# Performance work log

Hardware: AMD Instinct MI355X
Metric: run time of the kernel (lower is better)

Reference implementation:

```python
import jax, jax.numpy as jnp
import numpy as np

LMAX = 3
L2 = (LMAX + 1) ** 2
EPS = 1e-5
N_NODES = 2048
C_IN = 384
C_HID = 256


def _gaunt_tensor(lmax):
    # Real Gaunt coefficients G[i,j,k] = integral Y_i Y_j Y_k dOmega over S^2,
    # computed exactly with Gauss-Legendre (theta) x uniform (phi) quadrature.
    nt = 4 * lmax + 4
    nph = 8 * lmax + 8
    xg, wg = np.polynomial.legendre.leggauss(nt)
    ct, st = xg, np.sqrt(1.0 - xg ** 2)
    phi = 2.0 * np.pi * np.arange(nph) / nph
    # fully-normalized associated Legendre Pbar[l,m] on theta nodes
    P = np.zeros((lmax + 1, lmax + 1, nt))
    P[0, 0] = np.sqrt(1.0 / (4.0 * np.pi))
    for m in range(1, lmax + 1):
        P[m, m] = np.sqrt((2.0 * m + 1.0) / (2.0 * m)) * st * P[m - 1, m - 1]
    for m in range(lmax + 1):
        if m + 1 <= lmax:
            P[m + 1, m] = np.sqrt(2.0 * m + 3.0) * ct * P[m, m]
        for l in range(m + 2, lmax + 1):
            a = np.sqrt((4.0 * l * l - 1.0) / (l * l - m * m))
            b = np.sqrt(((l - 1.0) ** 2 - m * m) / (4.0 * (l - 1.0) ** 2 - 1.0))
            P[l, m] = a * (ct * P[l - 1, m] - b * P[l - 2, m])
    Y = np.zeros(((lmax + 1) ** 2, nt, nph))
    for l in range(lmax + 1):
        for m in range(-l, l + 1):
            idx = l * l + l + m
            if m == 0:
                Y[idx] = P[l, 0][:, None] * np.ones((1, nph))
            elif m > 0:
                Y[idx] = np.sqrt(2.0) * P[l, m][:, None] * np.cos(m * phi)[None, :]
            else:
                Y[idx] = np.sqrt(2.0) * P[l, -m][:, None] * np.sin(-m * phi)[None, :]
    W = wg[:, None] * (2.0 * np.pi / nph)  # [nt, nph]
    G = np.einsum('iap,jap,kap->ijk', Y, Y, Y * W[None])
    G[np.abs(G) < 1e-10] = 0.0
    return G


G_NP = _gaunt_tensor(LMAX)
SL = [slice(l * l, (l + 1) * (l + 1)) for l in range(LMAX + 1)]
_raw = []
for _l1 in range(LMAX + 1):
    for _l2 in range(LMAX + 1):
        for _l3 in range(LMAX + 1):
            _blk = G_NP[SL[_l1], SL[_l2], SL[_l3]]
            if np.abs(_blk).max() > 1e-8:
                _raw.append((_l1, _l2, _l3, _blk))
_fanin = {}
for _l1, _l2, _l3, _b in _raw:
    _fanin[_l3] = _fanin.get(_l3, 0) + 1
# component irrep normalization (sqrt(2l3+1)) and path normalization (1/sqrt(fan-in))
PATHS = [(l1, l2, l3, jnp.asarray((blk * np.sqrt(2.0 * l3 + 1.0) / np.sqrt(_fanin[l3])).astype(np.float32)))
         for (l1, l2, l3, blk) in _raw]
L_OF = jnp.asarray(np.repeat(np.arange(LMAX + 1), 2 * np.arange(LMAX + 1) + 1))  # [L2]


def setup_inputs() -> dict:
    key = jax.random.key(0)
    ks = jax.random.split(key, 9)
    inputs = jax.random.normal(ks[0], (N_NODES, L2, C_IN), jnp.float32)
    batch = jnp.sort(jax.random.randint(ks[1], (N_NODES,), 0, 64))
    norm_w = 1.0 + 0.1 * jax.random.normal(ks[2], (LMAX + 1, C_IN), jnp.float32)
    norm_b = 0.02 * jax.random.normal(ks[3], (C_IN,), jnp.float32)
    w1 = jax.random.normal(ks[4], (LMAX + 1, C_IN, C_HID), jnp.float32) / np.sqrt(C_IN)
    b1 = 0.02 * jax.random.normal(ks[5], (C_HID,), jnp.float32)
    w_gaunt = jax.random.normal(ks[6], (LMAX + 1, LMAX + 1, LMAX + 1, C_HID), jnp.float32)
    w2 = jax.random.normal(ks[7], (LMAX + 1, C_HID, C_IN), jnp.float32) / np.sqrt(C_HID)
    b2 = 0.02 * jax.random.normal(ks[8], (C_IN,), jnp.float32)
    return {"inputs": inputs, "batch": batch, "norm_w": norm_w, "norm_b": norm_b,
            "w1": w1, "b1": b1, "w_gaunt": w_gaunt, "w2": w2, "b2": b2}


def _forward(inputs, norm_w, norm_b, w1, b1, w_gaunt, w2, b2):
    # equivariant merge layer norm: center l=0 over channels, RMS over all (lm, C),
    # per-degree affine weight, bias on the l=0 (invariant) component only
    x = inputs
    x = x.at[:, 0, :].add(-jnp.mean(x[:, 0, :], axis=-1, keepdims=True))
    x = x * jax.lax.rsqrt(jnp.mean(x * x, axis=(1, 2), keepdims=True) + EPS)
    x = x * norm_w[L_OF][None]          # [N, L2, C]
    x = x.at[:, 0, :].add(norm_b)
    # SO3Linear 1: per-degree channel mixing, bias on l=0
    h = jnp.einsum('nic,ich->nih', x, w1[L_OF])
    h = h.at[:, 0, :].add(b1)
    # Gaunt depthwise self tensor product: per-channel CG-structured contraction
    t = jnp.zeros((inputs.shape[0], L2, w1.shape[-1]), dtype=h.dtype)
    for (l1, l2, l3, blk) in PATHS:
        hw = h[:, SL[l2], :] * w_gaunt[l1, l2, l3][None, None, :]     # [N, 2l2+1, H]
        tmp = jnp.einsum('ijk,nih->njkh', blk, h[:, SL[l1], :])       # small block contraction
        t = t.at[:, SL[l3], :].add(jnp.einsum('njkh,njh->nkh', tmp, hw))
    # SO3Linear 2
    out = jnp.einsum('nih,iho->nio', t, w2[L_OF])
    out = out.at[:, 0, :].add(b2)
    return out + inputs  # ffn_shortcut is Identity (num_in == num_out)


def reference(inputs, batch, norm_w, norm_b, w1, b1, w_gaunt, w2, b2):
    # drop_path / proj_drop are disabled (rates = 0); `batch` only feeds GraphDropPath
    return _forward(inputs, norm_w, norm_b, w1, b1, w_gaunt, w2, b2)
```

## Files before the change

kernel.cpp:

```cpp
#include <hip/hip_runtime.h>
#include <stdint.h>
#include <math.h>
#include <array>
#include <utility>

#ifndef M_PI
#define M_PI 3.14159265358979323846
#endif

#define NNODES 2048
#define L2DIM  16
#define CIN    384
#define CHID   256

typedef __attribute__((ext_vector_type(8))) short short8;
typedef __attribute__((ext_vector_type(4))) float f32x4;
typedef unsigned short u16;
typedef unsigned int   u32;

#define LOF(i) ((i) < 1 ? 0 : ((i) < 4 ? 1 : ((i) < 9 ? 2 : 3)))

static __device__ __forceinline__ u16 f2bf(float f) {
  u32 u = __builtin_bit_cast(u32, f);
  u = u + 0x7FFFu + ((u >> 16) & 1u);
  return (u16)(u >> 16);
}
static __device__ __forceinline__ float bf2f(u16 b) {
  u32 u = ((u32)b) << 16;
  return __builtin_bit_cast(float, u);
}

constexpr double CPI = 3.14159265358979323846;

constexpr double csqrt(double x) {
  if (x <= 0.0) return 0.0;
  double y = x > 1.0 ? x : 1.0;
  for (int i = 0; i < 48; ++i) y = 0.5 * (y + x / y);
  return y;
}
constexpr double ccos(double x) {
  double r = x;
  while (r > CPI)  r -= 2.0 * CPI;
  while (r < -CPI) r += 2.0 * CPI;
  double r2 = r * r, term = 1.0, sum = 1.0;
  for (int i = 1; i <= 26; ++i) { term *= -r2 / ((2.0 * i - 1.0) * (2.0 * i)); sum += term; }
  return sum;
}
constexpr int iabs_c(int x) { return x < 0 ? -x : x; }

struct GLQ { double x[16]; double w[16]; };
constexpr GLQ build_gl() {
  GLQ g{};
  const int n = 16;
  for (int i = 0; i < n; ++i) {
    double x = ccos(CPI * (i + 0.75) / (n + 0.5));
    double p1 = 0.0, dp = 1.0;
    for (int it = 0; it < 40; ++it) {
      double p0 = 1.0; p1 = x;
      for (int k = 2; k <= n; ++k) { double p2 = ((2.0*k-1.0)*x*p1 - (k-1.0)*p0)/k; p0 = p1; p1 = p2; }
      dp = n * (x*p1 - p0) / (x*x - 1.0);
      x -= p1 / dp;
    }
    { double p0 = 1.0; p1 = x;
      for (int k = 2; k <= n; ++k) { double p2 = ((2.0*k-1.0)*x*p1 - (k-1.0)*p0)/k; p0 = p1; p1 = p2; }
      dp = n * (x*p1 - p0) / (x*x - 1.0); }
    g.x[i] = x;
    g.w[i] = 2.0 / ((1.0 - x*x) * dp * dp);
  }
  return g;
}
constexpr GLQ QG = build_gl();

struct PTab { double v[4][4][16]; };
constexpr PTab build_pbar() {
  PTab T{};
  for (int t = 0; t < 16; ++t) {
    double ct = QG.x[t];
    double st = csqrt(1.0 - ct * ct);
    double P[4][4] = {};
    P[0][0] = csqrt(1.0 / (4.0 * CPI));
    for (int m = 1; m <= 3; ++m)
      P[m][m] = csqrt((2.0*m + 1.0) / (2.0*m)) * st * P[m-1][m-1];
    for (int m = 0; m <= 3; ++m) {
      if (m + 1 <= 3) P[m+1][m] = csqrt(2.0*m + 3.0) * ct * P[m][m];
      for (int l = m + 2; l <= 3; ++l) {
        double aa = csqrt((4.0*(double)l*l - 1.0) / ((double)l*l - (double)m*m));
        double bb = csqrt(((double)(l-1)*(l-1) - (double)m*m) / (4.0*(double)(l-1)*(l-1) - 1.0));
        P[l][m] = aa * (ct * P[l-1][m] - bb * P[l-2][m]);
      }
    }
    for (int l = 0; l < 4; ++l)
      for (int m = 0; m <= l; ++m) T.v[l][m][t] = P[l][m];
  }
  return T;
}
constexpr PTab PT = build_pbar();

constexpr double phi_int(int m1, int m2, int m3) {
  const double SQ2 = 1.41421356237309504880;
  int neg = (m1 < 0) + (m2 < 0) + (m3 < 0);
  if (neg & 1) return 0.0;
  int a = iabs_c(m1), b = iabs_c(m2), c = iabs_c(m3);
  int nz = (a > 0) + (b > 0) + (c > 0);
  if (nz == 0) return 2.0 * CPI;
  if (nz == 1) return 0.0;
  if (nz == 2) {
    int p = 0, q = 0;
    if (a == 0) { p = b; q = c; } else if (b == 0) { p = a; q = c; } else { p = a; q = b; }
    return (p == q) ? 2.0 * CPI : 0.0;
  }
  if (neg == 0) {
    double v = 0.0;
    if (iabs_c(a - b) == c && a != b) v += 1.0;
    if (a + b == c) v += 1.0;
    return SQ2 * CPI * v;
  }
  int p = 0, q = 0, r = 0;
  if (m1 > 0)      { p = a; q = b; r = c; }
  else if (m2 > 0) { p = b; q = a; r = c; }
  else             { p = c; q = a; r = b; }
  double v = 0.0;
  if (q != r && p == iabs_c(q - r)) v += 1.0;
  if (p == q + r) v -= 1.0;
  return SQ2 * CPI * v;
}

constexpr bool path_ok(int l1, int l2, int l3) {
  int lo = l1 > l2 ? l1 - l2 : l2 - l1;
  return l3 >= lo && l3 <= l1 + l2 && (((l1 + l2 + l3) & 1) == 0);
}
constexpr bool term_ok(int m1, int m2, int m3) {
  int aa = iabs_c(m1), bb = iabs_c(m2), cc = iabs_c(m3);
  int neg = (m1 < 0) + (m2 < 0) + (m3 < 0);
  if (neg & 1) return false;
  return (aa + bb == cc) || (bb + cc == aa) || (cc + aa == bb);
}
constexpr int count_paths() {
  int n = 0;
  for (int l1 = 0; l1 < 4; ++l1) for (int l2 = 0; l2 < 4; ++l2) for (int l3 = 0; l3 < 4; ++l3)
    if (path_ok(l1, l2, l3)) ++n;
  return n;
}
constexpr int NPATHS = count_paths();
constexpr int NTMAX  = 512;

constexpr double term_g(int l1, int m1, int l2, int m2, int l3, int m3) {
  double ph = phi_int(m1, m2, m3);
  if (ph == 0.0) return 0.0;
  int a = iabs_c(m1), b = iabs_c(m2), c = iabs_c(m3);
  double s = 0.0;
  for (int t = 0; t < 16; ++t)
    s += QG.w[t] * PT.v[l1][a][t] * PT.v[l2][b][t] * PT.v[l3][c][t];
  double g = ph * s;
  double fan = (l3 == 0) ? 4.0 : (l3 == 1 ? 6.0 : (l3 == 2 ? 7.0 : 6.0));
  return g * csqrt((2.0 * (double)l3 + 1.0) / fan);
}

struct TermG { float g; unsigned char i, j, k, p; };
struct PathT { unsigned char l1, l2, l3; };
struct TGAll { TermG t[NTMAX]; int n; };
constexpr TGAll build_all() {
  TGAll r{};
  r.n = 0;
  int p = 0;
  for (int l1 = 0; l1 < 4; ++l1) for (int l2 = 0; l2 < 4; ++l2) for (int l3 = 0; l3 < 4; ++l3) {
    if (!path_ok(l1, l2, l3)) continue;
    for (int m1 = -l1; m1 <= l1; ++m1) for (int m2 = -l2; m2 <= l2; ++m2) for (int m3 = -l3; m3 <= l3; ++m3) {
      if (!term_ok(m1, m2, m3)) continue;
      double g = term_g(l1, m1, l2, m2, l3, m3);
      if (g > 1e-10 || g < -1e-10) {
        r.t[r.n].g = (float)g;
        r.t[r.n].i = (unsigned char)(l1 * l1 + l1 + m1);
        r.t[r.n].j = (unsigned char)(l2 * l2 + l2 + m2);
        r.t[r.n].k = (unsigned char)(l3 * l3 + l3 + m3);
        r.t[r.n].p = (unsigned char)p;
        ++r.n;
      }
    }
    ++p;
  }
  return r;
}
constexpr TGAll TGA = build_all();
constexpr int NNZ = TGA.n;

constexpr std::array<PathT, NPATHS> build_paths() {
  std::array<PathT, NPATHS> a{};
  int n = 0;
  for (int l1 = 0; l1 < 4; ++l1) for (int l2 = 0; l2 < 4; ++l2) for (int l3 = 0; l3 < 4; ++l3)
    if (path_ok(l1, l2, l3)) a[n++] = PathT{(unsigned char)l1, (unsigned char)l2, (unsigned char)l3};
  return a;
}
constexpr auto PATHS_ARR = build_paths();

template <size_t... Is>
__device__ __forceinline__ void gaunt_terms(std::index_sequence<Is...>,
    float* __restrict__ t, const float* __restrict__ h,
    const float* __restrict__ wgv) {
  ((t[TGA.t[Is].k] = fmaf(TGA.t[Is].g * wgv[TGA.t[Is].p],
                          h[TGA.t[Is].i] * h[TGA.t[Is].j],
                          t[TGA.t[Is].k])), ...);
}
template <size_t... Ps>
__device__ __forceinline__ void load_wgv(std::index_sequence<Ps...>,
    float* __restrict__ wgv, const float* __restrict__ wg, int c) {
  ((wgv[Ps] = wg[(size_t)(((int)PATHS_ARR[Ps].l1 * 4 + (int)PATHS_ARR[Ps].l2) * 4
                          + (int)PATHS_ARR[Ps].l3) * CHID + c]), ...);
}

__global__ __launch_bounds__(256) void prep_kernel(
    const float* __restrict__ x, const float* __restrict__ nw,
    const float* __restrict__ nb, u16* __restrict__ xnb,
    const float* __restrict__ w1, const float* __restrict__ w2,
    u16* __restrict__ w1t, u16* __restrict__ w2t) {
  int bid = blockIdx.x, tid = threadIdx.x;
  if (bid >= NNODES) {
    __shared__ float tile[32][33];
    int b2 = bid - NNODES;
    int z = b2 / 144, rem = b2 % 144;
    int by = rem / 12, bx = rem % 12;
    int R = z < 4 ? 384 : 256, C = z < 4 ? 256 : 384;
    int r0 = by * 32, c0 = bx * 32;
    if (r0 >= R || c0 >= C) return;
    const float* s = (z < 4 ? w1 : w2) + (size_t)(z & 3) * R * C;
    u16* d = (z < 4 ? w1t : w2t) + (size_t)(z & 3) * R * C;
    int tx = tid & 31, ty = tid >> 5;
    for (int rr = ty; rr < 32; rr += 8)
      tile[rr][tx] = s[(size_t)(r0 + rr) * C + (c0 + tx)];
    __syncthreads();
    for (int cc = ty; cc < 32; cc += 8)
      d[(size_t)(c0 + cc) * R + (r0 + tx)] = f2bf(tile[tx][cc]);
    return;
  }
  int n = bid;
  const float* xr = x + (size_t)n * (L2DIM * CIN);
  __shared__ float2 red[4];
  float4 v[6];
  float ssq = 0.f, m0p = 0.f;
#pragma unroll
  for (int q = 0; q < 6; ++q) {
    v[q] = reinterpret_cast<const float4*>(xr)[tid * 6 + q];
    ssq += v[q].x*v[q].x + v[q].y*v[q].y + v[q].z*v[q].z + v[q].w*v[q].w;
  }
  if (tid < 16) {
#pragma unroll
    for (int q = 0; q < 6; ++q) m0p += v[q].x + v[q].y + v[q].z + v[q].w;
  }
  float a = m0p, b = ssq;
#pragma unroll
  for (int off = 32; off > 0; off >>= 1) { a += __shfl_down(a, off, 64); b += __shfl_down(b, off, 64); }
  int lane = tid & 63, wid = tid >> 6;
  if (lane == 0) red[wid] = make_float2(a, b);
  __syncthreads();
  float sum0 = red[0].x + red[1].x + red[2].x + red[3].x;
  float ssqt = red[0].y + red[1].y + red[2].y + red[3].y;
  float mean0 = sum0 * (1.0f / CIN);
  float ss = ssqt - (float)CIN * mean0 * mean0;
  float rstd = rsqrtf(ss * (1.0f / (L2DIM * CIN)) + 1e-5f);

  int lm = tid >> 4;
  int l = LOF(lm);
  bool row0 = (lm == 0);
  int cbase = (tid & 15) * 24;
  u16* orow = xnb + (size_t)n * (L2DIM * CIN) + (size_t)tid * 24;
#pragma unroll
  for (int q = 0; q < 6; ++q) {
    int c = cbase + q * 4;
    float4 w4 = *reinterpret_cast<const float4*>(&nw[l * CIN + c]);
    float4 b4 = row0 ? *reinterpret_cast<const float4*>(&nb[c]) : make_float4(0,0,0,0);
    float sub = row0 ? mean0 : 0.f;
    float o0 = (v[q].x - sub) * rstd * w4.x + b4.x;
    float o1 = (v[q].y - sub) * rstd * w4.y + b4.y;
    float o2 = (v[q].z - sub) * rstd * w4.z + b4.z;
    float o3 = (v[q].w - sub) * rstd * w4.w + b4.w;
    ushort4 pk;
    pk.x = f2bf(o0); pk.y = f2bf(o1); pk.z = f2bf(o2); pk.w = f2bf(o3);
    *reinterpret_cast<ushort4*>(&orow[q * 4]) = pk;
  }
}

template <int KD, int ND, int BN, bool SECOND>
__global__ __launch_bounds__(512) void so3_gemm_kernel(
    const u16* __restrict__ A, const u16* __restrict__ BT,
    const float* __restrict__ bias, const float* __restrict__ resid,
    u16* __restrict__ outb, float* __restrict__ outf) {
  constexpr int NFRAG = BN / 64;
  constexpr int WN_T = BN / 4;
  constexpr int KT = KD / 64;
  static_assert((BN % 64) == 0 && NFRAG * 16 == WN_T, "");
  int l = blockIdx.z;
  int twol1 = 2 * l + 1;
  int mtiles = (NNODES * twol1) >> 6;
  if ((int)blockIdx.x >= mtiles) return;
  int col0 = blockIdx.y * BN;
  int tid = threadIdx.x, lane = tid & 63, wid = tid >> 6;
  int wm = wid >> 2, wn = wid & 3;

  __shared__ u16 Asm[2][64 * 64];
  __shared__ u16 Bsm[2][BN * 64];

  int ar = tid >> 3;
  const u16* asrc;
  {
    int Rg = blockIdx.x * 64 + ar;
    int node = Rg / twol1;
    int lm = l * l + (Rg - node * twol1);
    asrc = A + (size_t)(node * L2DIM + lm) * KD + ((tid & 7) ^ (ar & 7)) * 8;
  }
  const u16* bsrc[BN / 64];
#pragma unroll
  for (int i = 0; i < BN / 64; ++i) {
    int r = i * 64 + (tid >> 3);
    bsrc[i] = BT + (size_t)(l * ND + col0 + r) * KD + ((tid & 7) ^ (r & 7)) * 8;
  }

  auto stage = [&](int buf, int kt) {
    __builtin_amdgcn_global_load_lds(
        (const __attribute__((address_space(1))) void*)(asrc + kt * 64),
        (__attribute__((address_space(3))) void*)(&Asm[buf][wid * 512]),
        16, 0, 0);
#pragma unroll
    for (int i = 0; i < BN / 64; ++i)
      __builtin_amdgcn_global_load_lds(
          (const __attribute__((address_space(1))) void*)(bsrc[i] + kt * 64),
          (__attribute__((address_space(3))) void*)(&Bsm[buf][i * 4096 + wid * 512]),
          16, 0, 0);
  };

  f32x4 acc[2][NFRAG];
#pragma unroll
  for (int i = 0; i < 2; ++i)
#pragma unroll
    for (int j = 0; j < NFRAG; ++j) acc[i][j] = (f32x4){0.f, 0.f, 0.f, 0.f};

  stage(0, 0);
  __syncthreads();
#pragma unroll
  for (int kt = 0; kt < KT; ++kt) {
    int cur = kt & 1;
    if (kt + 1 < KT) stage(cur ^ 1, kt + 1);
#pragma unroll
    for (int ks = 0; ks < 2; ++ks) {
      short8 af[2], bfv[NFRAG];
#pragma unroll
      for (int mf = 0; mf < 2; ++mf) {
        int row = wm * 32 + mf * 16 + (lane & 15);
        int slot = (ks * 4 + (lane >> 4)) ^ (row & 7);
        af[mf] = *reinterpret_cast<const short8*>(&Asm[cur][row * 64 + slot * 8]);
      }
#pragma unroll
      for (int nf = 0; nf < NFRAG; ++nf) {
        int brow = wn * WN_T + nf * 16 + (lane & 15);
        int slot = (ks * 4 + (lane >> 4)) ^ (brow & 7);
        bfv[nf] = *reinterpret_cast<const short8*>(&Bsm[cur][brow * 64 + slot * 8]);
      }
#pragma unroll
      for (int mf = 0; mf < 2; ++mf)
#pragma unroll
        for (int nf = 0; nf < NFRAG; ++nf)
          acc[mf][nf] = __builtin_amdgcn_mfma_f32_16x16x32_bf16(af[mf], bfv[nf], acc[mf][nf], 0, 0, 0);
    }
    __syncthreads();
  }

#pragma unroll
  for (int mf = 0; mf < 2; ++mf) {
#pragma unroll
    for (int jj = 0; jj < 4; ++jj) {
      int Rg = blockIdx.x * 64 + wm * 32 + mf * 16 + (lane >> 4) * 4 + jj;
      int node = Rg / twol1;
      int lm = l * l + (Rg - node * twol1);
      size_t rowoff = (size_t)(node * L2DIM + lm);
#pragma unroll
      for (int nf = 0; nf < NFRAG; ++nf) {
        int colg = col0 + wn * WN_T + nf * 16 + (lane & 15);
        float vv = acc[mf][nf][jj];
        if (l == 0) vv += bias[colg];
        if (!SECOND) {
          outb[rowoff * ND + colg] = f2bf(vv);
        } else {
          outf[rowoff * ND + colg] = vv + resid[rowoff * ND + colg];
        }
      }
    }
  }
}

__global__ __launch_bounds__(256, 2) void gaunt_kernel(
    const u16* __restrict__ hb, const float* __restrict__ wg,
    u16* __restrict__ tb) {
  int n = blockIdx.x, c = threadIdx.x;
  const u16* hr = hb + (size_t)n * (L2DIM * CHID) + c;
  float h[16];
#pragma unroll
  for (int i = 0; i < 16; ++i) h[i] = bf2f(hr[i * CHID]);

  float wgv[NPATHS];
  load_wgv(std::make_index_sequence<NPATHS>{}, wgv, wg, c);

  float t[16];
#pragma unroll
  for (int k = 0; k < 16; ++k) t[k] = 0.f;

  gaunt_terms(std::make_index_sequence<NNZ>{}, t, h, wgv);

  u16* tr = tb + (size_t)n * (L2DIM * CHID) + c;
#pragma unroll
  for (int k = 0; k < 16; ++k) tr[k * CHID] = f2bf(t[k]);
}

extern "C" void kernel_launch(void* const* d_in, const int* in_sizes, int n_in,
                              void* d_out, int out_size, void* d_ws, size_t ws_size,
                              hipStream_t stream) {
  const float* inputs = (const float*)d_in[0];
  const float* norm_w = (const float*)d_in[2];
  const float* norm_b = (const float*)d_in[3];
  const float* w1     = (const float*)d_in[4];
  const float* b1     = (const float*)d_in[5];
  const float* wga    = (const float*)d_in[6];
  const float* w2     = (const float*)d_in[7];
  const float* b2     = (const float*)d_in[8];
  float* out = (float*)d_out;

  uint8_t* ws = (uint8_t*)d_ws;
  u16*   w1t = (u16*)(ws + 16384);
  u16*   w2t = (u16*)(ws + 802816);
  u16*   xnb = (u16*)(ws + 1589248);
  u16*   tb  = xnb;
  u16*   hb  = (u16*)(ws + 26755072);

  prep_kernel<<<NNODES + 1152, 256, 0, stream>>>(
      inputs, norm_w, norm_b, xnb, w1, w2, w1t, w2t);
  so3_gemm_kernel<CIN, CHID, 256, false><<<dim3(224, 1, 4), 512, 0, stream>>>(
      xnb, w1t, b1, nullptr, hb, nullptr);
  gaunt_kernel<<<NNODES, 256, 0, stream>>>(hb, wga, tb);
  so3_gemm_kernel<CHID, CIN, 192, true><<<dim3(224, 2, 4), 512, 0, stream>>>(
      tb, w2t, b2, inputs, nullptr, out);
}
```

Baseline: 86.82 us.

## Stage GEMM epilogue through LDS for vectorized stores; widen gaunt to two channels

The GEMM epilogue now writes accumulators into an LDS tile that reuses the staging buffers, then each thread writes contiguous row segments with 16-byte vector stores, adding the bias and residual as float4 values. The old epilogue issued scattered 2- or 4-byte stores. Separately, the gaunt kernel now processes two channels per thread with 32-bit loads and stores and float2 weight loads, which halves the grid. This cuts the number of memory transactions at the cost of one extra barrier, more LDS in the epilogue, and higher register pressure in the gaunt kernel (its occupancy launch bound was removed).

```diff
diff --git a/kernel.cpp b/kernel.cpp
--- a/kernel.cpp
+++ b/kernel.cpp
@@ -202,10 +202,14 @@
                           t[TGA.t[Is].k])), ...);
 }
 template <size_t... Ps>
-__device__ __forceinline__ void load_wgv(std::index_sequence<Ps...>,
-    float* __restrict__ wgv, const float* __restrict__ wg, int c) {
-  ((wgv[Ps] = wg[(size_t)(((int)PATHS_ARR[Ps].l1 * 4 + (int)PATHS_ARR[Ps].l2) * 4
-                          + (int)PATHS_ARR[Ps].l3) * CHID + c]), ...);
+__device__ __forceinline__ void load_wgv2(std::index_sequence<Ps...>,
+    float* __restrict__ w0, float* __restrict__ w1,
+    const float* __restrict__ wg, int c) {
+  float2 tmp;
+  (((tmp = *reinterpret_cast<const float2*>(
+        &wg[(size_t)(((int)PATHS_ARR[Ps].l1 * 4 + (int)PATHS_ARR[Ps].l2) * 4
+                     + (int)PATHS_ARR[Ps].l3) * CHID + c]),
+     w0[Ps] = tmp.x, w1[Ps] = tmp.y)), ...);
 }
 
 __global__ __launch_bounds__(256) void prep_kernel(
@@ -287,7 +291,12 @@
   constexpr int NFRAG = BN / 64;
   constexpr int WN_T = BN / 4;
   constexpr int KT = KD / 64;
+  constexpr int EPSS = BN + 8;
+  constexpr int SMEM_STAGE = 16384 + 2 * BN * 64 * 2;
+  constexpr int SMEM_EPI = 64 * EPSS * 4;
+  constexpr int SMEM = SMEM_STAGE > SMEM_EPI ? SMEM_STAGE : SMEM_EPI;
   static_assert((BN % 64) == 0 && NFRAG * 16 == WN_T, "");
+
   int l = blockIdx.z;
   int twol1 = 2 * l + 1;
   int mtiles = (NNODES * twol1) >> 6;
@@ -296,8 +305,10 @@
   int tid = threadIdx.x, lane = tid & 63, wid = tid >> 6;
   int wm = wid >> 2, wn = wid & 3;
 
-  __shared__ u16 Asm[2][64 * 64];
-  __shared__ u16 Bsm[2][BN * 64];
+  __shared__ __align__(16) char smem[SMEM];
+  u16* AsmB = (u16*)smem;
+  u16* BsmB = (u16*)(smem + 16384);
+  float* eps = (float*)smem;
 
   int ar = tid >> 3;
   const u16* asrc;
@@ -317,13 +328,13 @@
   auto stage = [&](int buf, int kt) {
     __builtin_amdgcn_global_load_lds(
         (const __attribute__((address_space(1))) void*)(asrc + kt * 64),
-        (__attribute__((address_space(3))) void*)(&Asm[buf][wid * 512]),
+        (__attribute__((address_space(3))) void*)(&AsmB[buf * 4096 + wid * 512]),
         16, 0, 0);
 #pragma unroll
     for (int i = 0; i < BN / 64; ++i)
       __builtin_amdgcn_global_load_lds(
           (const __attribute__((address_space(1))) void*)(bsrc[i] + kt * 64),
-          (__attribute__((address_space(3))) void*)(&Bsm[buf][i * 4096 + wid * 512]),
+          (__attribute__((address_space(3))) void*)(&BsmB[buf * (BN * 64) + i * 4096 + wid * 512]),
           16, 0, 0);
   };
 
@@ -346,13 +357,13 @@
       for (int mf = 0; mf < 2; ++mf) {
         int row = wm * 32 + mf * 16 + (lane & 15);
         int slot = (ks * 4 + (lane >> 4)) ^ (row & 7);
-        af[mf] = *reinterpret_cast<const short8*>(&Asm[cur][row * 64 + slot * 8]);
+        af[mf] = *reinterpret_cast<const short8*>(&AsmB[cur * 4096 + row * 64 + slot * 8]);
       }
 #pragma unroll
       for (int nf = 0; nf < NFRAG; ++nf) {
         int brow = wn * WN_T + nf * 16 + (lane & 15);
         int slot = (ks * 4 + (lane >> 4)) ^ (brow & 7);
-        bfv[nf] = *reinterpret_cast<const short8*>(&Bsm[cur][brow * 64 + slot * 8]);
+        bfv[nf] = *reinterpret_cast<const short8*>(&BsmB[cur * (BN * 64) + brow * 64 + slot * 8]);
       }
 #pragma unroll
       for (int mf = 0; mf < 2; ++mf)
@@ -364,49 +375,91 @@
   }
 
 #pragma unroll
-  for (int mf = 0; mf < 2; ++mf) {
-#pragma unroll
-    for (int jj = 0; jj < 4; ++jj) {
-      int Rg = blockIdx.x * 64 + wm * 32 + mf * 16 + (lane >> 4) * 4 + jj;
-      int node = Rg / twol1;
-      int lm = l * l + (Rg - node * twol1);
-      size_t rowoff = (size_t)(node * L2DIM + lm);
-#pragma unroll
-      for (int nf = 0; nf < NFRAG; ++nf) {
-        int colg = col0 + wn * WN_T + nf * 16 + (lane & 15);
-        float vv = acc[mf][nf][jj];
-        if (l == 0) vv += bias[colg];
-        if (!SECOND) {
-          outb[rowoff * ND + colg] = f2bf(vv);
-        } else {
-          outf[rowoff * ND + colg] = vv + resid[rowoff * ND + colg];
-        }
-      }
-    }
-  }
-}
-
-__global__ __launch_bounds__(256, 2) void gaunt_kernel(
+  for (int mf = 0; mf < 2; ++mf)
+#pragma unroll
+    for (int nf = 0; nf < NFRAG; ++nf)
+#pragma unroll
+      for (int jj = 0; jj < 4; ++jj) {
+        int row = wm * 32 + mf * 16 + (lane >> 4) * 4 + jj;
+        int col = wn * WN_T + nf * 16 + (lane & 15);
+        eps[row * EPSS + col] = acc[mf][nf][jj];
+      }
+  __syncthreads();
+
+  constexpr int CPT = BN / 8;
+  int r = tid >> 3, cb = (tid & 7) * CPT;
+  int Rg = blockIdx.x * 64 + r;
+  int node = Rg / twol1;
+  int lm = l * l + (Rg - node * twol1);
+  size_t base = (size_t)(node * L2DIM + lm) * ND + col0 + cb;
+
+  if (!SECOND) {
+    u16* og = outb + base;
+#pragma unroll
+    for (int q = 0; q < CPT / 8; ++q) {
+      float4 a = *reinterpret_cast<const float4*>(&eps[r * EPSS + cb + q * 8]);
+      float4 b = *reinterpret_cast<const float4*>(&eps[r * EPSS + cb + q * 8 + 4]);
+      if (l == 0) {
+        float4 ba = *reinterpret_cast<const float4*>(&bias[col0 + cb + q * 8]);
+        float4 bb = *reinterpret_cast<const float4*>(&bias[col0 + cb + q * 8 + 4]);
+        a.x += ba.x; a.y += ba.y; a.z += ba.z; a.w += ba.w;
+        b.x += bb.x; b.y += bb.y; b.z += bb.z; b.w += bb.w;
+      }
+      u32 p0 = (u32)f2bf(a.x) | ((u32)f2bf(a.y) << 16);
+      u32 p1 = (u32)f2bf(a.z) | ((u32)f2bf(a.w) << 16);
+      u32 p2 = (u32)f2bf(b.x) | ((u32)f2bf(b.y) << 16);
+      u32 p3 = (u32)f2bf(b.z) | ((u32)f2bf(b.w) << 16);
+      uint4 pk = make_uint4(p0, p1, p2, p3);
+      *reinterpret_cast<uint4*>(&og[q * 8]) = pk;
+    }
+  } else {
+    float* og = outf + base;
+    const float* rg = resid + base;
+#pragma unroll
+    for (int q = 0; q < CPT / 4; ++q) {
+      float4 v = *reinterpret_cast<const float4*>(&eps[r * EPSS + cb + q * 4]);
+      if (l == 0) {
+        float4 ba = *reinterpret_cast<const float4*>(&bias[col0 + cb + q * 4]);
+        v.x += ba.x; v.y += ba.y; v.z += ba.z; v.w += ba.w;
+      }
+      float4 rv = *reinterpret_cast<const float4*>(&rg[q * 4]);
+      v.x += rv.x; v.y += rv.y; v.z += rv.z; v.w += rv.w;
+      *reinterpret_cast<float4*>(&og[q * 4]) = v;
+    }
+  }
+}
+
+__global__ __launch_bounds__(256) void gaunt_kernel(
     const u16* __restrict__ hb, const float* __restrict__ wg,
     u16* __restrict__ tb) {
-  int n = blockIdx.x, c = threadIdx.x;
+  int tid = threadIdx.x;
+  int n = blockIdx.x * 2 + (tid >> 7);
+  int c = (tid & 127) * 2;
   const u16* hr = hb + (size_t)n * (L2DIM * CHID) + c;
-  float h[16];
-#pragma unroll
-  for (int i = 0; i < 16; ++i) h[i] = bf2f(hr[i * CHID]);
-
-  float wgv[NPATHS];
-  load_wgv(std::make_index_sequence<NPATHS>{}, wgv, wg, c);
-
-  float t[16];
-#pragma unroll
-  for (int k = 0; k < 16; ++k) t[k] = 0.f;
-
-  gaunt_terms(std::make_index_sequence<NNZ>{}, t, h, wgv);
+  float h0[16], h1[16];
+#pragma unroll
+  for (int i = 0; i < 16; ++i) {
+    u32 w = *reinterpret_cast<const u32*>(&hr[i * CHID]);
+    h0[i] = bf2f((u16)(w & 0xffffu));
+    h1[i] = bf2f((u16)(w >> 16));
+  }
+
+  float w0[NPATHS], w1[NPATHS];
+  load_wgv2(std::make_index_sequence<NPATHS>{}, w0, w1, wg, c);
+
+  float t0[16], t1[16];
+#pragma unroll
+  for (int k = 0; k < 16; ++k) { t0[k] = 0.f; t1[k] = 0.f; }
+
+  gaunt_terms(std::make_index_sequence<NNZ>{}, t0, h0, w0);
+  gaunt_terms(std::make_index_sequence<NNZ>{}, t1, h1, w1);
 
   u16* tr = tb + (size_t)n * (L2DIM * CHID) + c;
 #pragma unroll
-  for (int k = 0; k < 16; ++k) tr[k * CHID] = f2bf(t[k]);
+  for (int k = 0; k < 16; ++k) {
+    u32 o = (u32)f2bf(t0[k]) | ((u32)f2bf(t1[k]) << 16);
+    *reinterpret_cast<u32*>(&tr[k * CHID]) = o;
+  }
 }
 
 extern "C" void kernel_launch(void* const* d_in, const int* in_sizes, int n_in,
@@ -433,7 +486,7 @@
       inputs, norm_w, norm_b, xnb, w1, w2, w1t, w2t);
   so3_gemm_kernel<CIN, CHID, 256, false><<<dim3(224, 1, 4), 512, 0, stream>>>(
       xnb, w1t, b1, nullptr, hb, nullptr);
-  gaunt_kernel<<<NNODES, 256, 0, stream>>>(hb, wga, tb);
+  gaunt_kernel<<<NNODES / 2, 256, 0, stream>>>(hb, wga, tb);
   so3_gemm_kernel<CHID, CIN, 192, true><<<dim3(224, 2, 4), 512, 0, stream>>>(
       tb, w2t, b2, inputs, nullptr, out);
 }
```

Result: slower. 121.5 us (+39.9%).
